# Kernel optimization log

Hardware: AMD Instinct MI355X
Metric: run time of the kernel (lower is better)

## Reference

```python
import jax, jax.numpy as jnp
import numpy as np

EMBED = 256
HEADS = 8
LEVELS = 1
POINTS = 4
HEAD_DIM = EMBED // HEADS  # 32
SPATIAL = [(200, 200)]     # static (H, W) per level
BS = 2
NQ = 40000
NV = sum(h * w for h, w in SPATIAL)


def setup_inputs() -> dict:
    key = jax.random.key(0)
    ks = jax.random.split(key, 12)
    s = 0.02
    inp = {
        "query": jax.random.normal(ks[0], (BS, NQ, EMBED), jnp.float32),
        "value": jax.random.normal(ks[1], (BS, NV, EMBED), jnp.float32),
        "reference_points": jax.random.uniform(ks[2], (BS, NQ, LEVELS, 2), jnp.float32),
        "spatial_shapes": jnp.array(SPATIAL, dtype=jnp.int32),
        "W_value": jax.random.normal(ks[3], (EMBED, EMBED), jnp.float32) * s,
        "b_value": jax.random.normal(ks[4], (EMBED,), jnp.float32) * s,
        "W_off": jax.random.normal(ks[5], (EMBED, HEADS * LEVELS * POINTS * 2), jnp.float32) * s,
        "b_off": jax.random.normal(ks[6], (HEADS * LEVELS * POINTS * 2,), jnp.float32) * s,
        "W_attn": jax.random.normal(ks[7], (EMBED, HEADS * LEVELS * POINTS), jnp.float32) * s,
        "b_attn": jax.random.normal(ks[8], (HEADS * LEVELS * POINTS,), jnp.float32) * s,
        "W_out": jax.random.normal(ks[9], (EMBED, EMBED), jnp.float32) * s,
        "b_out": jax.random.normal(ks[10], (EMBED,), jnp.float32) * s,
    }
    return inp


def _bilinear_sample(v_l, x, y, H, W):
    """grid_sample(bilinear, padding zeros, align_corners=False) on flat spatial.
    v_l: [bs, heads, H*W, d]; x, y: [bs, nq, heads, P] pixel coords.
    Returns [bs, nq, heads, P, d]."""
    bs = v_l.shape[0]
    nq = x.shape[1]
    x0 = jnp.floor(x)
    y0 = jnp.floor(y)
    out = jnp.zeros((bs, nq, HEADS, POINTS, HEAD_DIM), v_l.dtype)
    for dx in (0, 1):
        for dy in (0, 1):
            xi = x0 + dx
            yi = y0 + dy
            w = (1.0 - jnp.abs(x - xi)) * (1.0 - jnp.abs(y - yi))
            valid = (xi >= 0) & (xi <= W - 1) & (yi >= 0) & (yi <= H - 1)
            xi_c = jnp.clip(xi, 0, W - 1).astype(jnp.int32)
            yi_c = jnp.clip(yi, 0, H - 1).astype(jnp.int32)
            idx = yi_c * W + xi_c                               # [bs,nq,heads,P]
            idx = idx.transpose(0, 2, 1, 3).reshape(bs, HEADS, nq * POINTS)
            g = jnp.take_along_axis(v_l, idx[..., None], axis=2)  # [bs,heads,nq*P,d]
            g = g.reshape(bs, HEADS, nq, POINTS, HEAD_DIM).transpose(0, 2, 1, 3, 4)
            out = out + g * (w * valid.astype(w.dtype))[..., None]
    return out


def reference(query, value, reference_points, spatial_shapes,
              W_value, b_value, W_off, b_off, W_attn, b_attn, W_out, b_out):
    bs, nq, _ = query.shape
    # value projection
    v = (value @ W_value + b_value).reshape(bs, -1, HEADS, HEAD_DIM)
    v = v.transpose(0, 2, 1, 3)  # [bs, heads, nv, d]
    # sampling offsets and attention weights from query
    off = (query @ W_off + b_off).reshape(bs, nq, HEADS, LEVELS, POINTS, 2)
    aw = (query @ W_attn + b_attn).reshape(bs, nq, HEADS, LEVELS * POINTS)
    aw = jax.nn.softmax(aw, axis=-1).reshape(bs, nq, HEADS, LEVELS, POINTS)
    # sampling locations in [0,1] (reference_points last dim == 2 branch)
    normalizer = jnp.stack([spatial_shapes[:, 1], spatial_shapes[:, 0]], -1).astype(query.dtype)  # [L,2]=(W,H)
    loc = reference_points[:, :, None, :, None, :] + off / normalizer[None, None, None, :, None, :]
    out = jnp.zeros((bs, nq, HEADS, HEAD_DIM), query.dtype)
    start = 0
    for lvl, (H, W) in enumerate(SPATIAL):
        v_l = v[:, :, start:start + H * W]            # [bs,heads,HW,d]
        g = 2.0 * loc[:, :, :, lvl] - 1.0             # [bs,nq,heads,P,2] in [-1,1]
        px = ((g[..., 0] + 1.0) * W - 1.0) / 2.0      # align_corners=False
        py = ((g[..., 1] + 1.0) * H - 1.0) / 2.0
        sampled = _bilinear_sample(v_l, px, py, H, W)  # [bs,nq,heads,P,d]
        out = out + (sampled * aw[:, :, :, lvl, :, None]).sum(axis=3)
        start += H * W
    out = out.reshape(bs, nq, EMBED) @ W_out + b_out
    # dropout is identity in eval; identity residual = query (no query_pos)
    return out + query
```

## Files before the change

kernel.cpp:

```cpp
#include <hip/hip_runtime.h>


typedef float  f4  __attribute__((ext_vector_type(4)));
typedef float  fx4 __attribute__((ext_vector_type(4)));
typedef short  s8  __attribute__((ext_vector_type(8)));
typedef short  s4  __attribute__((ext_vector_type(4)));

#define KDIM    256
#define NVPIX   40000
#define GH      200
#define GW      200
#define LDP     68

__device__ __forceinline__ short f2bf(float f) {
  union { float f; unsigned u; } v; v.f = f;
  unsigned r = v.u + 0x7fffu + ((v.u >> 16) & 1u);
  return (short)(r >> 16);
}
__device__ __forceinline__ float bf2f(unsigned short h) {
  union { unsigned u; float f; } v; v.u = ((unsigned)h) << 16; return v.f;
}

__global__ void prep_k(const float* __restrict__ Wv, const float* __restrict__ Wo,
                       const float* __restrict__ Woff, const float* __restrict__ Wattn,
                       const float* __restrict__ boff, const float* __restrict__ battn,
                       unsigned short* __restrict__ Wv_t, unsigned short* __restrict__ Wo_t,
                       unsigned short* __restrict__ Wp_t, float* __restrict__ bp)
{
  int i = blockIdx.x * 256 + threadIdx.x;
  if (i < 65536) {
    int n = i >> 8, k = i & 255;
    Wv_t[i] = (unsigned short)f2bf(Wv[k * 256 + n]);
  } else if (i < 131072) {
    int j = i - 65536; int n = j >> 8, k = j & 255;
    Wo_t[j] = (unsigned short)f2bf(Wo[k * 256 + n]);
  } else if (i < 163840) {
    int j = i - 131072; int n = j >> 8, k = j & 255;
    float val = (n < 64) ? Woff[k * 64 + n] : ((n < 96) ? Wattn[k * 32 + (n - 64)] : 0.f);
    Wp_t[j] = (unsigned short)f2bf(val);
  } else if (i < 163968) {
    int j = i - 163840;
    bp[j] = (j < 64) ? boff[j] : ((j < 96) ? battn[j - 64] : 0.f);
  }
}

template<int ABF, int CBF, int RES>
__global__ __launch_bounds__(256)
void gemm_k(const void* __restrict__ Ap, const unsigned short* __restrict__ Bt,
            const float* __restrict__ bias, const float* __restrict__ resid,
            void* __restrict__ Cp, int N)
{
  __shared__ short As[128 * LDP];
  __shared__ short Bs[128 * LDP];
  const int t  = threadIdx.x;
  const int m0 = blockIdx.x * 128;
  const int n0 = blockIdx.y * 128;
  const int lane = t & 63;
  const int w  = t >> 6;
  const int wm = (w >> 1) * 64;
  const int wn = (w & 1) * 64;
  const int fr = lane & 15;
  const int quad = lane >> 4;

  fx4 acc[4][4];
  #pragma unroll
  for (int i = 0; i < 4; i++)
    #pragma unroll
    for (int j = 0; j < 4; j++) { fx4 z = {0.f, 0.f, 0.f, 0.f}; acc[i][j] = z; }

  f4 pa[8];
  s8 pa8[4];
  s8 pb[4];

  auto loadA = [&](int k0) {
    if (ABF) {
      const unsigned short* base = (const unsigned short*)Ap + (size_t)m0 * KDIM + k0;
      #pragma unroll
      for (int j = 0; j < 4; j++) {
        int id = t + j * 256;
        int row = id >> 3, kp = (id & 7) * 8;
        pa8[j] = *(const s8*)(base + (size_t)row * KDIM + kp);
      }
    } else {
      const float* base = (const float*)Ap + (size_t)m0 * KDIM + k0;
      #pragma unroll
      for (int j = 0; j < 8; j++) {
        int id = t + j * 256;
        int row = id >> 4, kp = (id & 15) * 4;
        pa[j] = *(const f4*)(base + (size_t)row * KDIM + kp);
      }
    }
  };
  auto loadB = [&](int k0) {
    const unsigned short* base = Bt + (size_t)n0 * KDIM + k0;
    #pragma unroll
    for (int j = 0; j < 4; j++) {
      int id = t + j * 256;
      int row = id >> 3, kp = (id & 7) * 8;
      pb[j] = *(const s8*)(base + (size_t)row * KDIM + kp);
    }
  };
  auto storeAB = [&]() {
    if (ABF) {
      #pragma unroll
      for (int j = 0; j < 4; j++) {
        int id = t + j * 256;
        int row = id >> 3, kp = (id & 7) * 8;
        *(s8*)(&As[row * LDP + kp]) = pa8[j];
      }
    } else {
      #pragma unroll
      for (int j = 0; j < 8; j++) {
        int id = t + j * 256;
        int row = id >> 4, kp = (id & 15) * 4;
        s4 c;
        #pragma unroll
        for (int e = 0; e < 4; e++) c[e] = f2bf(pa[j][e]);
        *(s4*)(&As[row * LDP + kp]) = c;
      }
    }
    #pragma unroll
    for (int j = 0; j < 4; j++) {
      int id = t + j * 256;
      int row = id >> 3, kp = (id & 7) * 8;
      *(s8*)(&Bs[row * LDP + kp]) = pb[j];
    }
  };

  loadA(0); loadB(0);
  #pragma unroll
  for (int it = 0; it < 4; ++it) {
    __syncthreads();
    storeAB();
    __syncthreads();
    if (it < 3) { loadA((it + 1) * 64); loadB((it + 1) * 64); }
    #pragma unroll
    for (int kk = 0; kk < 2; kk++) {
      s8 afr[4], bfr[4];
      #pragma unroll
      for (int i = 0; i < 4; i++)
        afr[i] = *(const s8*)(&As[(wm + i * 16 + fr) * LDP + kk * 32 + quad * 8]);
      #pragma unroll
      for (int i = 0; i < 4; i++)
        bfr[i] = *(const s8*)(&Bs[(wn + i * 16 + fr) * LDP + kk * 32 + quad * 8]);
      #pragma unroll
      for (int i = 0; i < 4; i++)
        #pragma unroll
        for (int j = 0; j < 4; j++)
          acc[i][j] = __builtin_amdgcn_mfma_f32_16x16x32_bf16(afr[i], bfr[j], acc[i][j], 0, 0, 0);
    }
  }

  #pragma unroll
  for (int i = 0; i < 4; i++) {
    const int mbase = m0 + wm + i * 16 + quad * 4;
    #pragma unroll
    for (int j = 0; j < 4; j++) {
      const int n = n0 + wn + j * 16 + fr;
      const float bn = bias[n];
      #pragma unroll
      for (int r = 0; r < 4; r++) {
        const size_t m = (size_t)(mbase + r);
        float v = acc[i][j][r] + bn;
        if (RES) v += resid[m * (size_t)N + n];
        if (CBF) ((unsigned short*)Cp)[m * (size_t)N + n] = (unsigned short)f2bf(v);
        else     ((float*)Cp)[m * (size_t)N + n] = v;
      }
    }
  }
}

__global__ __launch_bounds__(256)
void sample_k(const unsigned short* __restrict__ v, const float* __restrict__ p,
              const float* __restrict__ ref, unsigned short* __restrict__ o)
{
  const int t  = threadIdx.x;
  const int q0 = blockIdx.x * 8;
  __shared__ float sp[8][128];
  __shared__ float sref[16];
  {
    const float* pb = p + (size_t)q0 * 128;
    #pragma unroll
    for (int j = 0; j < 4; j++) {
      int i = t + j * 256;
      sp[i >> 7][i & 127] = pb[i];
    }
    if (t < 16) sref[t] = ref[(size_t)q0 * 2 + t];
  }
  __syncthreads();

  const int qi = t >> 5;
  const int h  = (t >> 2) & 7;
  const int dg = t & 3;
  const int q  = q0 + qi;
  const int b  = (q >= 40000) ? 1 : 0;

  const float lg0 = sp[qi][64 + h * 4 + 0], lg1 = sp[qi][64 + h * 4 + 1];
  const float lg2 = sp[qi][64 + h * 4 + 2], lg3 = sp[qi][64 + h * 4 + 3];
  const float mx = fmaxf(fmaxf(lg0, lg1), fmaxf(lg2, lg3));
  const float e0 = __expf(lg0 - mx), e1 = __expf(lg1 - mx);
  const float e2 = __expf(lg2 - mx), e3 = __expf(lg3 - mx);
  const float inv = 1.f / (e0 + e1 + e2 + e3);
  const float aws[4] = {e0 * inv, e1 * inv, e2 * inv, e3 * inv};
  const float rx = sref[qi * 2], ry = sref[qi * 2 + 1];

  const unsigned short* vb = v + (size_t)b * NVPIX * 256;
  const int cbase = h * 32 + dg * 8;

  float acc[8];
  #pragma unroll
  for (int e = 0; e < 8; e++) acc[e] = 0.f;

  #pragma unroll
  for (int pt = 0; pt < 4; ++pt) {
    const float ox = sp[qi][h * 8 + pt * 2], oy = sp[qi][h * 8 + pt * 2 + 1];
    const float px = rx * 200.f + ox - 0.5f;
    const float py = ry * 200.f + oy - 0.5f;
    const float x0f = floorf(px), y0f = floorf(py);
    const int ix = (int)x0f, iy = (int)y0f;
    const float fx = px - x0f, fy = py - y0f;
    const float a = aws[pt];
    const float vx0 = (ix >= 0 && ix < GW) ? 1.f : 0.f;
    const float vx1 = (ix + 1 >= 0 && ix + 1 < GW) ? 1.f : 0.f;
    const float vy0 = (iy >= 0 && iy < GH) ? 1.f : 0.f;
    const float vy1 = (iy + 1 >= 0 && iy + 1 < GH) ? 1.f : 0.f;
    const float w00 = a * (1.f - fx) * (1.f - fy) * vx0 * vy0;
    const float w01 = a * fx * (1.f - fy) * vx1 * vy0;
    const float w10 = a * (1.f - fx) * fy * vx0 * vy1;
    const float w11 = a * fx * fy * vx1 * vy1;
    const int ix0c = min(max(ix, 0), GW - 1);
    const int ix1c = min(max(ix + 1, 0), GW - 1);
    const int iy0c = min(max(iy, 0), GH - 1);
    const int iy1c = min(max(iy + 1, 0), GH - 1);
    const int r0 = iy0c * (GW * 256) + cbase;
    const int r1 = iy1c * (GW * 256) + cbase;
    s8 g00 = *(const s8*)(vb + r0 + ix0c * 256);
    s8 g01 = *(const s8*)(vb + r0 + ix1c * 256);
    s8 g10 = *(const s8*)(vb + r1 + ix0c * 256);
    s8 g11 = *(const s8*)(vb + r1 + ix1c * 256);
    #pragma unroll
    for (int e = 0; e < 8; e++) {
      acc[e] += w00 * bf2f((unsigned short)g00[e]) + w01 * bf2f((unsigned short)g01[e])
              + w10 * bf2f((unsigned short)g10[e]) + w11 * bf2f((unsigned short)g11[e]);
    }
  }

  s8 res;
  #pragma unroll
  for (int e = 0; e < 8; e++) res[e] = f2bf(acc[e]);
  *(s8*)(o + (size_t)q * 256 + cbase) = res;
}

extern "C" void kernel_launch(void* const* d_in, const int* in_sizes, int n_in,
                              void* d_out, int out_size, void* d_ws, size_t ws_size,
                              hipStream_t stream)
{
  const float* query = (const float*)d_in[0];
  const float* value = (const float*)d_in[1];
  const float* refp  = (const float*)d_in[2];
  const float* Wv    = (const float*)d_in[4];
  const float* bv    = (const float*)d_in[5];
  const float* Woff  = (const float*)d_in[6];
  const float* boff  = (const float*)d_in[7];
  const float* Wattn = (const float*)d_in[8];
  const float* battn = (const float*)d_in[9];
  const float* Wo    = (const float*)d_in[10];
  const float* bo    = (const float*)d_in[11];

  char* ws = (char*)d_ws;
  unsigned short* ws_v = (unsigned short*)ws;
  float*          ws_p = (float*)(ws + 40960000);
  unsigned short* ws_o = (unsigned short*)(ws + 81920000);
  unsigned short* Wv_t = (unsigned short*)(ws + 122880000);
  unsigned short* Wo_t = Wv_t + 65536;
  unsigned short* Wp_t = Wo_t + 65536;
  float*          bp   = (float*)(Wp_t + 32768);

  hipLaunchKernelGGL(prep_k, dim3(641), dim3(256), 0, stream,
                     Wv, Wo, Woff, Wattn, boff, battn, Wv_t, Wo_t, Wp_t, bp);
  hipLaunchKernelGGL((gemm_k<0, 1, 0>), dim3(625, 2), dim3(256), 0, stream,
                     (const void*)value, Wv_t, bv, (const float*)nullptr, (void*)ws_v, 256);
  hipLaunchKernelGGL((gemm_k<0, 0, 0>), dim3(625, 1), dim3(256), 0, stream,
                     (const void*)query, Wp_t, bp, (const float*)nullptr, (void*)ws_p, 128);
  hipLaunchKernelGGL(sample_k, dim3(10000), dim3(256), 0, stream,
                     ws_v, ws_p, refp, ws_o);
  hipLaunchKernelGGL((gemm_k<1, 0, 1>), dim3(625, 2), dim3(256), 0, stream,
                     (const void*)ws_o, Wo_t, bo, query, (void*)d_out, 256);
}
```

Baseline: 354.8 us.

## Widen GEMM tiles to full N with 512-thread blocks, cap sample_k occupancy

```diff
diff --git a/kernel.cpp b/kernel.cpp
--- a/kernel.cpp
+++ b/kernel.cpp
@@ -44,58 +44,59 @@
   }
 }
 
-template<int ABF, int CBF, int RES>
-__global__ __launch_bounds__(256)
+template<int ABF, int CBF, int RES, int BN>
+__global__ __launch_bounds__(512)
 void gemm_k(const void* __restrict__ Ap, const unsigned short* __restrict__ Bt,
             const float* __restrict__ bias, const float* __restrict__ resid,
-            void* __restrict__ Cp, int N)
-{
+            void* __restrict__ Cp)
+{
+  constexpr int ACCJ = BN / 64;
+  constexpr int WN   = BN / 4;
   __shared__ short As[128 * LDP];
-  __shared__ short Bs[128 * LDP];
+  __shared__ short Bs[BN * LDP];
   const int t  = threadIdx.x;
   const int m0 = blockIdx.x * 128;
-  const int n0 = blockIdx.y * 128;
   const int lane = t & 63;
   const int w  = t >> 6;
-  const int wm = (w >> 1) * 64;
-  const int wn = (w & 1) * 64;
+  const int wm = (w >> 2) * 64;
+  const int wn = (w & 3) * WN;
   const int fr = lane & 15;
   const int quad = lane >> 4;
 
-  fx4 acc[4][4];
+  fx4 acc[4][ACCJ];
   #pragma unroll
   for (int i = 0; i < 4; i++)
     #pragma unroll
-    for (int j = 0; j < 4; j++) { fx4 z = {0.f, 0.f, 0.f, 0.f}; acc[i][j] = z; }
-
-  f4 pa[8];
-  s8 pa8[4];
-  s8 pb[4];
+    for (int j = 0; j < ACCJ; j++) { fx4 z = {0.f, 0.f, 0.f, 0.f}; acc[i][j] = z; }
+
+  f4 pa[4];
+  s8 pa8[2];
+  s8 pb[ACCJ];
 
   auto loadA = [&](int k0) {
     if (ABF) {
       const unsigned short* base = (const unsigned short*)Ap + (size_t)m0 * KDIM + k0;
       #pragma unroll
-      for (int j = 0; j < 4; j++) {
-        int id = t + j * 256;
+      for (int j = 0; j < 2; j++) {
+        int id = t + j * 512;
         int row = id >> 3, kp = (id & 7) * 8;
         pa8[j] = *(const s8*)(base + (size_t)row * KDIM + kp);
       }
     } else {
       const float* base = (const float*)Ap + (size_t)m0 * KDIM + k0;
       #pragma unroll
-      for (int j = 0; j < 8; j++) {
-        int id = t + j * 256;
+      for (int j = 0; j < 4; j++) {
+        int id = t + j * 512;
         int row = id >> 4, kp = (id & 15) * 4;
         pa[j] = *(const f4*)(base + (size_t)row * KDIM + kp);
       }
     }
   };
   auto loadB = [&](int k0) {
-    const unsigned short* base = Bt + (size_t)n0 * KDIM + k0;
-    #pragma unroll
-    for (int j = 0; j < 4; j++) {
-      int id = t + j * 256;
+    const unsigned short* base = Bt + k0;
+    #pragma unroll
+    for (int j = 0; j < ACCJ; j++) {
+      int id = t + j * 512;
       int row = id >> 3, kp = (id & 7) * 8;
       pb[j] = *(const s8*)(base + (size_t)row * KDIM + kp);
     }
@@ -103,15 +104,15 @@
   auto storeAB = [&]() {
     if (ABF) {
       #pragma unroll
-      for (int j = 0; j < 4; j++) {
-        int id = t + j * 256;
+      for (int j = 0; j < 2; j++) {
+        int id = t + j * 512;
         int row = id >> 3, kp = (id & 7) * 8;
         *(s8*)(&As[row * LDP + kp]) = pa8[j];
       }
     } else {
       #pragma unroll
-      for (int j = 0; j < 8; j++) {
-        int id = t + j * 256;
+      for (int j = 0; j < 4; j++) {
+        int id = t + j * 512;
         int row = id >> 4, kp = (id & 15) * 4;
         s4 c;
         #pragma unroll
@@ -120,8 +121,8 @@
       }
     }
     #pragma unroll
-    for (int j = 0; j < 4; j++) {
-      int id = t + j * 256;
+    for (int j = 0; j < ACCJ; j++) {
+      int id = t + j * 512;
       int row = id >> 3, kp = (id & 7) * 8;
       *(s8*)(&Bs[row * LDP + kp]) = pb[j];
     }
@@ -136,17 +137,17 @@
     if (it < 3) { loadA((it + 1) * 64); loadB((it + 1) * 64); }
     #pragma unroll
     for (int kk = 0; kk < 2; kk++) {
-      s8 afr[4], bfr[4];
+      s8 afr[4], bfr[ACCJ];
       #pragma unroll
       for (int i = 0; i < 4; i++)
         afr[i] = *(const s8*)(&As[(wm + i * 16 + fr) * LDP + kk * 32 + quad * 8]);
       #pragma unroll
-      for (int i = 0; i < 4; i++)
-        bfr[i] = *(const s8*)(&Bs[(wn + i * 16 + fr) * LDP + kk * 32 + quad * 8]);
+      for (int j = 0; j < ACCJ; j++)
+        bfr[j] = *(const s8*)(&Bs[(wn + j * 16 + fr) * LDP + kk * 32 + quad * 8]);
       #pragma unroll
       for (int i = 0; i < 4; i++)
         #pragma unroll
-        for (int j = 0; j < 4; j++)
+        for (int j = 0; j < ACCJ; j++)
           acc[i][j] = __builtin_amdgcn_mfma_f32_16x16x32_bf16(afr[i], bfr[j], acc[i][j], 0, 0, 0);
     }
   }
@@ -155,22 +156,22 @@
   for (int i = 0; i < 4; i++) {
     const int mbase = m0 + wm + i * 16 + quad * 4;
     #pragma unroll
-    for (int j = 0; j < 4; j++) {
-      const int n = n0 + wn + j * 16 + fr;
+    for (int j = 0; j < ACCJ; j++) {
+      const int n = wn + j * 16 + fr;
       const float bn = bias[n];
       #pragma unroll
       for (int r = 0; r < 4; r++) {
         const size_t m = (size_t)(mbase + r);
         float v = acc[i][j][r] + bn;
-        if (RES) v += resid[m * (size_t)N + n];
-        if (CBF) ((unsigned short*)Cp)[m * (size_t)N + n] = (unsigned short)f2bf(v);
-        else     ((float*)Cp)[m * (size_t)N + n] = v;
-      }
-    }
-  }
-}
-
-__global__ __launch_bounds__(256)
+        if (RES) v += resid[m * (size_t)BN + n];
+        if (CBF) ((unsigned short*)Cp)[m * (size_t)BN + n] = (unsigned short)f2bf(v);
+        else     ((float*)Cp)[m * (size_t)BN + n] = v;
+      }
+    }
+  }
+}
+
+__global__ __launch_bounds__(256, 8)
 void sample_k(const unsigned short* __restrict__ v, const float* __restrict__ p,
               const float* __restrict__ ref, unsigned short* __restrict__ o)
 {
@@ -278,12 +279,12 @@
 
   hipLaunchKernelGGL(prep_k, dim3(641), dim3(256), 0, stream,
                      Wv, Wo, Woff, Wattn, boff, battn, Wv_t, Wo_t, Wp_t, bp);
-  hipLaunchKernelGGL((gemm_k<0, 1, 0>), dim3(625, 2), dim3(256), 0, stream,
-                     (const void*)value, Wv_t, bv, (const float*)nullptr, (void*)ws_v, 256);
-  hipLaunchKernelGGL((gemm_k<0, 0, 0>), dim3(625, 1), dim3(256), 0, stream,
-                     (const void*)query, Wp_t, bp, (const float*)nullptr, (void*)ws_p, 128);
+  hipLaunchKernelGGL((gemm_k<0, 1, 0, 256>), dim3(625), dim3(512), 0, stream,
+                     (const void*)value, Wv_t, bv, (const float*)nullptr, (void*)ws_v);
+  hipLaunchKernelGGL((gemm_k<0, 0, 0, 128>), dim3(625), dim3(512), 0, stream,
+                     (const void*)query, Wp_t, bp, (const float*)nullptr, (void*)ws_p);
   hipLaunchKernelGGL(sample_k, dim3(10000), dim3(256), 0, stream,
                      ws_v, ws_p, refp, ws_o);
-  hipLaunchKernelGGL((gemm_k<1, 0, 1>), dim3(625, 2), dim3(256), 0, stream,
-                     (const void*)ws_o, Wo_t, bo, query, (void*)d_out, 256);
-}
+  hipLaunchKernelGGL((gemm_k<1, 0, 1, 256>), dim3(625), dim3(512), 0, stream,
+                     (const void*)ws_o, Wo_t, bo, query, (void*)d_out);
+}
```

After: 628.4 us. 1.77x slower.
